# Optimization experiments

Hardware: AMD Instinct MI355X
Metric: run time of the kernel (lower is better)

The kernel has to match this reference:

```python
import jax, jax.numpy as jnp
import numpy as np

SEQ, D, HID, C = 512, 768, 128, 5
NENT, SPAN = 128, 16


def setup_inputs() -> dict:
    key = jax.random.key(0)
    ks = jax.random.split(key, 24)
    s = 0.02

    def rn(k, shape, scale=s):
        return jax.random.normal(k, shape, dtype=jnp.float32) * scale

    inp = {
        "encoder_output": rn(ks[0], (1, SEQ, D), 1.0),
        "holder_idxs": jax.random.randint(ks[1], (NENT, SPAN), 0, SEQ, dtype=jnp.int32),
        "target_idxs": jax.random.randint(ks[2], (NENT, SPAN), 0, SEQ, dtype=jnp.int32),
        "exp_idxs": jax.random.randint(ks[3], (NENT, SPAN), 0, SEQ, dtype=jnp.int32),
    }
    names = ["Wh_f", "bh_f", "Wh_b", "bh_b", "Wt_f", "bt_f", "Wt_b", "bt_b",
             "We_f", "be_f", "We_b", "be_b"]
    for n, k in zip(names, ks[4:16]):
        shape = (4 * HID, D) if n.startswith("W") else (4 * HID,)
        inp[n] = rn(k, shape)
    inp["T_he"] = rn(ks[16], (2 * HID, 2 * HID, 2 * HID))
    inp["T_te"] = rn(ks[17], (2 * HID, 2 * HID, 2 * HID))
    inp["T_cls"] = rn(ks[18], (2 * HID, C, 2 * HID))
    return inp


def _lstm_cell_step(x, W_ih, b):
    # Single LSTM step with h0=c0=0 (the torch module feeds seq_len=1 to nn.LSTM,
    # so W_hh @ h0 vanishes; b = b_ih + b_hh). Gate order: i, f, g, o.
    g = x @ W_ih.T + b                         # [n, L, 4H]
    i, f, gg, o = jnp.split(g, 4, axis=-1)
    c = jax.nn.sigmoid(i) * jnp.tanh(gg)
    return jax.nn.sigmoid(o) * jnp.tanh(c)     # h, [n, L, H]


def _lstm_pool(enc_seq, idxs, Wf, bf, Wb, bb):
    toks = enc_seq[idxs]                       # [n, L, D] gather
    h = jnp.concatenate([_lstm_cell_step(toks, Wf, bf),
                         _lstm_cell_step(toks, Wb, bb)], axis=-1)  # [n, L, 2H]
    return h.max(axis=1)                       # max-pool over span -> [n, 2H]


def reference(encoder_output, holder_idxs, target_idxs, exp_idxs,
              Wh_f, bh_f, Wh_b, bh_b, Wt_f, bt_f, Wt_b, bt_b,
              We_f, be_f, We_b, be_b, T_he, T_te, T_cls):
    enc = encoder_output[0]                    # [SEQ, D]
    He = _lstm_pool(enc, holder_idxs, Wh_f, bh_f, Wh_b, bh_b)   # [nh, 2H]
    Te = _lstm_pool(enc, target_idxs, Wt_f, bt_f, Wt_b, bt_b)   # [nt, 2H]
    Ee = _lstm_pool(enc, exp_idxs, We_f, be_f, We_b, be_b)      # [ne, 2H]

    # hep[i,k] = He[i] @ T_he @ Ee[k];  tep[j,k] = Te[j] @ T_te @ Ee[k]
    hep = jnp.einsum('ia,abc,kc->ikb', He, T_he, Ee)            # [nh, ne, 2H]
    tep = jnp.einsum('ja,abc,kc->jkb', Te, T_te, Ee)            # [nt, ne, 2H]
    # pred[i,j,k,m] = tep[j,k] @ T_cls[:,m,:] @ hep[i,k]
    pred = jnp.einsum('jkb,bmc,ikc->ijkm', tep, T_cls, hep)     # [nh, nt, ne, C]
    return pred
```

## Files before the change

kernel.cpp:

```cpp
#include <hip/hip_runtime.h>
#include <hip/hip_bf16.h>
#include <math.h>

#define DIM   768
#define HID   128
#define H2    256
#define NENT  128
#define SPAN  16
#define NCLS  5

#define POOLB_OFF  0
#define HEPB_OFF   196608
#define TEPB_OFF   (HEPB_OFF + 8388608)
#define TCLSB_OFF  (TEPB_OFF + 8388608)
#define WB_OFF     (TCLSB_OFF + 655360)
#define TOKB_OFF   21168128
#define TMP30_OFF  21168128
#define TMP31_OFF  (TMP30_OFF + 16777216)
#define GATESB_OFF 58060800
#define PREDT_OFF  21168128

typedef __attribute__((ext_vector_type(8))) short bf16x8;
typedef __attribute__((ext_vector_type(4))) float f32x4;

__device__ __forceinline__ float sigmoidf_(float x) { return 1.0f / (1.0f + __expf(-x)); }

__device__ __forceinline__ unsigned short f2bf(float x) {
    __hip_bfloat16 h = __float2bfloat16(x);
    return *reinterpret_cast<unsigned short*>(&h);
}
__device__ __forceinline__ float bf2f(unsigned short u) {
    unsigned int v = ((unsigned int)u) << 16;
    float f; __builtin_memcpy(&f, &v, 4); return f;
}

__global__ __launch_bounds__(256)
void prep_kernel(const float* __restrict__ Whf, const float* __restrict__ Whb,
                 const float* __restrict__ Wtf, const float* __restrict__ Wtb,
                 const float* __restrict__ Wef, const float* __restrict__ Web,
                 const float* __restrict__ Tcls, const float* __restrict__ enc,
                 const int* __restrict__ idx_h, const int* __restrict__ idx_t,
                 const int* __restrict__ idx_e,
                 unsigned short* __restrict__ WB, unsigned short* __restrict__ TB,
                 unsigned short* __restrict__ tokB)
{
    const int bb = blockIdx.x;
    const int tid = threadIdx.x;
    if (bb < 1728) {
        int gid = bb * 256 + tid;
        int t2  = gid / 73728;
        int rem = gid % 73728;
        int n   = rem / 192;
        int c4  = rem % 192;
        int gate = n >> 7, j = n & 127;
        int srow = (gate == 0) ? j : (gate == 1) ? 256 + j : 384 + j;
        const float* W = (t2 == 0) ? Whf : (t2 == 1) ? Whb : (t2 == 2) ? Wtf :
                         (t2 == 3) ? Wtb : (t2 == 4) ? Wef : Web;
        float4 v = ((const float4*)(W + srow * DIM))[c4];
        unsigned short* d = WB + ((size_t)(t2 * 384 + n)) * DIM + c4 * 4;
        d[0] = f2bf(v.x); d[1] = f2bf(v.y); d[2] = f2bf(v.z); d[3] = f2bf(v.w);
    } else if (bb < 3008) {
        int idx = (bb - 1728) * 256 + tid;
        int b = idx / (NCLS * H2);
        int r = idx % (NCLS * H2);
        int m = r >> 8, c = r & 255;
        TB[((m << 8) + c) * H2 + b] = f2bf(Tcls[idx]);
    } else {
        int gid = (bb - 3008) * 256 + tid;
        int r  = gid / 192, c4 = gid % 192;
        int type = r >> 11;
        int rem  = r & 2047;
        const int* idx = (type == 0) ? idx_h : (type == 1) ? idx_t : idx_e;
        int row = idx[rem];
        float4 v = ((const float4*)(enc + (size_t)row * DIM))[c4];
        unsigned short h4[4] = { f2bf(v.x), f2bf(v.y), f2bf(v.z), f2bf(v.w) };
        *(uint2*)(tokB + (size_t)r * DIM + c4 * 4) = *(uint2*)h4;
    }
}

__global__ __launch_bounds__(256)
void gates_mfma(const unsigned short* __restrict__ tokB,
                const unsigned short* __restrict__ WB,
                unsigned short* __restrict__ gatesB)
{
    __shared__ unsigned short As[2][128 * 64];
    __shared__ unsigned short Bs[2][128 * 64];
    const int lbid = ((int)blockIdx.x & 7) * 36 + ((int)blockIdx.x >> 3);
    const int type = lbid / 96;
    const int rem  = lbid % 96;
    const int mb0  = (rem / 6) * 128;
    const int nb0  = (rem % 6) * 128;
    const int tid = threadIdx.x;
    const int w = tid >> 6, l = tid & 63;
    const int lr = l & 15, lg = l >> 4;
    const unsigned short* A = tokB + (size_t)type * 2048 * DIM + (size_t)mb0 * DIM;
    const unsigned short* B = WB   + (size_t)type * 768  * DIM + (size_t)nb0 * DIM;

    const int sr0 = tid >> 3;
    const int sc  = tid & 7;

    bf16x8 ra[4], rb[4];
    #define LOADT(kt)                                                        \
        {                                                                    \
            const int koff = (kt) * 64 + sc * 8;                             \
            _Pragma("unroll")                                                \
            for (int p = 0; p < 4; ++p) {                                    \
                int rr = sr0 + p * 32;                                       \
                ra[p] = *(const bf16x8*)(A + (size_t)rr * DIM + koff);       \
                rb[p] = *(const bf16x8*)(B + (size_t)rr * DIM + koff);       \
            }                                                                \
        }
    #define WRITET(buf)                                                      \
        {                                                                    \
            _Pragma("unroll")                                                \
            for (int p = 0; p < 4; ++p) {                                    \
                int rr = sr0 + p * 32;                                       \
                int bo = (rr * 128 + sc * 16) ^ ((rr & 7) << 4);             \
                *(bf16x8*)((char*)As[buf] + bo) = ra[p];                     \
                *(bf16x8*)((char*)Bs[buf] + bo) = rb[p];                     \
            }                                                                \
        }

    f32x4 acc[4][4];
    #pragma unroll
    for (int mt = 0; mt < 4; ++mt)
        #pragma unroll
        for (int nt = 0; nt < 4; ++nt) acc[mt][nt] = (f32x4){0.f, 0.f, 0.f, 0.f};

    const int am0 = (w & 1) * 64;
    const int bn0 = (w >> 1) * 64;

    LOADT(0);
    WRITET(0);
    __syncthreads();

    int cur = 0;
    #pragma unroll 1
    for (int kt = 0; kt < 12; ++kt) {
        if (kt + 1 < 12) LOADT(kt + 1);

        #pragma unroll
        for (int ks = 0; ks < 2; ++ks) {
            bf16x8 af[4], bf[4];
            #pragma unroll
            for (int mt = 0; mt < 4; ++mt) {
                int rr = am0 + mt * 16 + lr;
                int bo = (rr * 128 + ks * 64 + lg * 16) ^ ((rr & 7) << 4);
                af[mt] = *(const bf16x8*)((const char*)As[cur] + bo);
            }
            #pragma unroll
            for (int nt = 0; nt < 4; ++nt) {
                int rr = bn0 + nt * 16 + lr;
                int bo = (rr * 128 + ks * 64 + lg * 16) ^ ((rr & 7) << 4);
                bf[nt] = *(const bf16x8*)((const char*)Bs[cur] + bo);
            }
            #pragma unroll
            for (int mt = 0; mt < 4; ++mt)
                #pragma unroll
                for (int nt = 0; nt < 4; ++nt)
                    acc[mt][nt] = __builtin_amdgcn_mfma_f32_16x16x32_bf16(af[mt], bf[nt], acc[mt][nt], 0, 0, 0);
        }

        if (kt + 1 < 12) {
            WRITET(cur ^ 1);
        }
        __syncthreads();
        cur ^= 1;
    }
    #undef LOADT
    #undef WRITET

    unsigned short* C = gatesB + (size_t)type * 2048 * 768 + (size_t)mb0 * 768 + nb0;
    #pragma unroll
    for (int mt = 0; mt < 4; ++mt)
        #pragma unroll
        for (int nt = 0; nt < 4; ++nt)
            #pragma unroll
            for (int r = 0; r < 4; ++r)
                C[(size_t)(am0 + mt * 16 + lg * 4 + r) * 768 + bn0 + nt * 16 + lr] = f2bf(acc[mt][nt][r]);
}

__global__ __launch_bounds__(256)
void pool_epilogue(const unsigned short* __restrict__ gatesB,
                   const float* __restrict__ bhf, const float* __restrict__ bhb,
                   const float* __restrict__ btf, const float* __restrict__ btb,
                   const float* __restrict__ bef, const float* __restrict__ beb,
                   unsigned short* __restrict__ poolB)
{
    const int type = blockIdx.x >> 7;
    const int ent  = blockIdx.x & 127;
    const int tid  = threadIdx.x;
    const int dir  = tid >> 7;
    const int j    = tid & 127;
    const float* Bv = (type == 0) ? (dir ? bhb : bhf)
                    : (type == 1) ? (dir ? btb : btf)
                                  : (dir ? beb : bef);
    const float bi = Bv[j], bg = Bv[2 * HID + j], bo = Bv[3 * HID + j];
    const unsigned short* g0 = gatesB + ((size_t)type * 2048 + ent * 16) * 768 + dir * 384 + j;
    float hmax = -1e30f;
    #pragma unroll
    for (int ll = 0; ll < SPAN; ++ll) {
        const unsigned short* gr = g0 + ll * 768;
        float iv = sigmoidf_(bf2f(gr[0])   + bi);
        float gv = tanhf(   bf2f(gr[128]) + bg);
        float ov = sigmoidf_(bf2f(gr[256]) + bo);
        hmax = fmaxf(hmax, ov * tanhf(iv * gv));
    }
    poolB[(size_t)(type * NENT + ent) * H2 + dir * HID + j] = f2bf(hmax);
}

__global__ __launch_bounds__(256)
void p1_thin(const unsigned short* __restrict__ EeB,
             const float* __restrict__ T0, const float* __restrict__ T1,
             unsigned short* __restrict__ tmp30, unsigned short* __restrict__ tmp31)
{
    __shared__ __align__(16) char smem[32768];
    const int bid = blockIdx.x;
    const int t  = bid >> 10;
    const int b  = (bid >> 2) & 255;
    const int aq = bid & 3;
    const int a0 = aq * 64;
    const float* T = t ? T1 : T0;
    unsigned short* outp = t ? tmp31 : tmp30;
    const int tid = threadIdx.x;
    const int w = tid >> 6, l = tid & 63;
    const int lr = l & 15, lg = l >> 4;

    #pragma unroll
    for (int p = 0; p < 8; ++p) {
        int L = tid + p * 256;
        int row = L >> 5, ch = L & 31;
        const float* src = T + ((size_t)(a0 + row) * 256 + b) * 256 + ch * 8;
        float4 v0 = ((const float4*)src)[0];
        float4 v1 = ((const float4*)src)[1];
        bf16x8 hv; unsigned short* hp = (unsigned short*)&hv;
        hp[0]=f2bf(v0.x); hp[1]=f2bf(v0.y); hp[2]=f2bf(v0.z); hp[3]=f2bf(v0.w);
        hp[4]=f2bf(v1.x); hp[5]=f2bf(v1.y); hp[6]=f2bf(v1.z); hp[7]=f2bf(v1.w);
        int bo = (((ch >> 3) << 13) + row * 128 + ((ch & 7) << 4)) ^ ((row & 7) << 4);
        *(bf16x8*)(smem + bo) = hv;
    }
    __syncthreads();

    const int aw = (w & 1) * 32;
    const int kw = (w >> 1) * 64;
    f32x4 acc[2][4];
    #pragma unroll
    for (int mt = 0; mt < 2; ++mt)
        #pragma unroll
        for (int nt = 0; nt < 4; ++nt) acc[mt][nt] = (f32x4){0.f, 0.f, 0.f, 0.f};

    #pragma unroll
    for (int ks = 0; ks < 8; ++ks) {
        const int cb = ks * 64 + lg * 16;
        bf16x8 af[2], bf[4];
        #pragma unroll
        for (int mt = 0; mt < 2; ++mt) {
            int row = aw + mt * 16 + lr;
            int bo = (((cb >> 7) << 13) + row * 128 + (cb & 127)) ^ ((row & 7) << 4);
            af[mt] = *(const bf16x8*)(smem + bo);
        }
        #pragma unroll
        for (int nt = 0; nt < 4; ++nt)
            bf[nt] = *(const bf16x8*)(EeB + (kw + nt * 16 + lr) * H2 + ks * 32 + lg * 8);
        #pragma unroll
        for (int mt = 0; mt < 2; ++mt)
            #pragma unroll
            for (int nt = 0; nt < 4; ++nt)
                acc[mt][nt] = __builtin_amdgcn_mfma_f32_16x16x32_bf16(af[mt], bf[nt], acc[mt][nt], 0, 0, 0);
    }

    #pragma unroll
    for (int mt = 0; mt < 2; ++mt)
        #pragma unroll
        for (int nt = 0; nt < 4; ++nt)
            #pragma unroll
            for (int r = 0; r < 4; ++r) {
                int a_ = a0 + aw + mt * 16 + lg * 4 + r;
                int k_ = kw + nt * 16 + lr;
                outp[((size_t)b * 256 + a_) * 128 + k_] = f2bf(acc[mt][nt][r]);
            }
}

__global__ __launch_bounds__(512)
void gemm2_mfma(const unsigned short* __restrict__ HeB, const unsigned short* __restrict__ TeB,
                const unsigned short* __restrict__ tmp30, const unsigned short* __restrict__ tmp31,
                unsigned short* __restrict__ hepN, unsigned short* __restrict__ tepN)
{
    __shared__ unsigned short WT[128 * 256];
    const int bid = blockIdx.x;
    const int t = bid >> 8;
    const int b = bid & 255;
    const unsigned short* src = (t ? tmp31 : tmp30) + (size_t)b * 32768;
    const unsigned short* Hx = t ? TeB : HeB;
    unsigned short* outp = (t ? tepN : hepN) + (size_t)b * 16384;
    const int tid = threadIdx.x;
    const int w = tid >> 6, l = tid & 63;
    const int lr = l & 15, lg = l >> 4;

    {
        const int a0 = tid >> 4;
        const int k8 = (tid & 15) * 8;
        #pragma unroll
        for (int it = 0; it < 8; ++it) {
            int aa = it * 32 + a0;
            bf16x8 v = *(const bf16x8*)(src + aa * 128 + k8);
            #pragma unroll
            for (int j = 0; j < 8; ++j) {
                int kk = k8 + j;
                int bo = (kk * 512 + aa * 2) ^ (j << 4);
                *(unsigned short*)((char*)WT + bo) = ((unsigned short*)&v)[j];
            }
        }
    }
    __syncthreads();

    const int kw = (w & 1) * 64;
    const int iw = (w >> 1) * 32;
    f32x4 acc[4][2];
    #pragma unroll
    for (int mt = 0; mt < 4; ++mt)
        #pragma unroll
        for (int nt = 0; nt < 2; ++nt) acc[mt][nt] = (f32x4){0.f, 0.f, 0.f, 0.f};

    #pragma unroll
    for (int ks = 0; ks < 8; ++ks) {
        bf16x8 af[4], bf[2];
        #pragma unroll
        for (int mt = 0; mt < 4; ++mt) {
            int kr = kw + mt * 16 + lr;
            int bo = (kr * 512 + (ks * 32 + lg * 8) * 2) ^ ((kr & 7) << 4);
            af[mt] = *(const bf16x8*)((const char*)WT + bo);
        }
        #pragma unroll
        for (int nt = 0; nt < 2; ++nt)
            bf[nt] = *(const bf16x8*)(Hx + (iw + nt * 16 + lr) * H2 + ks * 32 + lg * 8);
        #pragma unroll
        for (int mt = 0; mt < 4; ++mt)
            #pragma unroll
            for (int nt = 0; nt < 2; ++nt)
                acc[mt][nt] = __builtin_amdgcn_mfma_f32_16x16x32_bf16(af[mt], bf[nt], acc[mt][nt], 0, 0, 0);
    }
    #pragma unroll
    for (int mt = 0; mt < 4; ++mt)
        #pragma unroll
        for (int nt = 0; nt < 2; ++nt)
            #pragma unroll
            for (int r = 0; r < 4; ++r) {
                int k_ = kw + mt * 16 + lg * 4 + r;
                int i_ = iw + nt * 16 + lr;
                outp[k_ * 128 + i_] = f2bf(acc[mt][nt][r]);
            }
}

__global__ __launch_bounds__(512)
void step3_mfma(const unsigned short* __restrict__ hepN,
                const unsigned short* __restrict__ tepN,
                const unsigned short* __restrict__ TclsB,
                float* __restrict__ predT)
{
    __shared__ unsigned short hepS[128 * 256];
    __shared__ unsigned short tepS[64 * 256];
    __shared__ unsigned short WS[64 * 256];
    const int lbid = (blockIdx.x & 7) * 32 + (blockIdx.x >> 3);
    const int k  = lbid >> 1;
    const int jh = lbid & 1;
    const int tid = threadIdx.x;
    const int w  = tid >> 6;
    const int l  = tid & 63;
    const int lr = l & 15;
    const int lg = l >> 4;
    const int swz = (lr & 7) << 4;

    #pragma unroll
    for (int q = 0; q < 4; ++q) {
        int bcol = q * 64 + l;
        bf16x8 v = *(const bf16x8*)(tepN + ((size_t)bcol * 128 + k) * 128 + jh * 64 + w * 8);
        #pragma unroll
        for (int r = 0; r < 8; ++r) {
            int j = w * 8 + r;
            int bo = (j * 512 + bcol * 2) ^ (r << 4);
            *(unsigned short*)((char*)tepS + bo) = ((unsigned short*)&v)[r];
        }
    }
    #pragma unroll
    for (int s = 0; s < 2; ++s)
        #pragma unroll
        for (int q = 0; q < 4; ++q) {
            int bcol = q * 64 + l;
            bf16x8 v = *(const bf16x8*)(hepN + ((size_t)bcol * 128 + k) * 128 + w * 16 + s * 8);
            #pragma unroll
            for (int r = 0; r < 8; ++r) {
                int i = w * 16 + s * 8 + r;
                int bo = (i * 512 + bcol * 2) ^ (r << 4);
                *(unsigned short*)((char*)hepS + bo) = ((unsigned short*)&v)[r];
            }
        }
    __syncthreads();

    bf16x8 ha[8];
    #pragma unroll
    for (int ks = 0; ks < 8; ++ks) {
        int ir = w * 16 + lr;
        int bo = (ir * 512 + (ks * 32 + lg * 8) * 2) ^ ((ir & 7) << 4);
        ha[ks] = *(const bf16x8*)((const char*)hepS + bo);
    }

    #pragma unroll 1
    for (int m = 0; m < NCLS; ++m) {
        {
            const unsigned short* tcm = TclsB + (size_t)m * (H2 * H2);
            f32x4 acc1[4][2];
            #pragma unroll
            for (int jt = 0; jt < 4; ++jt)
                #pragma unroll
                for (int ct = 0; ct < 2; ++ct) acc1[jt][ct] = (f32x4){0.f, 0.f, 0.f, 0.f};

            #pragma unroll
            for (int ks = 0; ks < 8; ++ks) {
                bf16x8 a[4], bb[2];
                #pragma unroll
                for (int jt = 0; jt < 4; ++jt) {
                    int byteoff = ((((jt * 16 + lr) << 8) + ks * 32 + lg * 8) << 1) ^ swz;
                    a[jt] = *(const bf16x8*)((const char*)tepS + byteoff);
                }
                #pragma unroll
                for (int ct = 0; ct < 2; ++ct)
                    bb[ct] = *(const bf16x8*)(tcm + (size_t)(w * 32 + ct * 16 + lr) * H2 + ks * 32 + lg * 8);
                #pragma unroll
                for (int jt = 0; jt < 4; ++jt)
                    #pragma unroll
                    for (int ct = 0; ct < 2; ++ct)
                        acc1[jt][ct] = __builtin_amdgcn_mfma_f32_16x16x32_bf16(a[jt], bb[ct], acc1[jt][ct], 0, 0, 0);
            }
            #pragma unroll
            for (int jt = 0; jt < 4; ++jt)
                #pragma unroll
                for (int ct = 0; ct < 2; ++ct)
                    #pragma unroll
                    for (int r = 0; r < 4; ++r) {
                        int j = jt * 16 + lg * 4 + r;
                        int c = w * 32 + ct * 16 + lr;
                        int byteoff = ((((j << 8) + c)) << 1) ^ ((j & 7) << 4);
                        *(unsigned short*)((char*)WS + byteoff) = f2bf(acc1[jt][ct][r]);
                    }
        }
        __syncthreads();

        {
            f32x4 acc2[4];
            #pragma unroll
            for (int jt = 0; jt < 4; ++jt) acc2[jt] = (f32x4){0.f, 0.f, 0.f, 0.f};

            #pragma unroll
            for (int ks = 0; ks < 8; ++ks) {
                #pragma unroll
                for (int jt = 0; jt < 4; ++jt) {
                    int byteoff = ((((jt * 16 + lr) << 8) + ks * 32 + lg * 8) << 1) ^ swz;
                    bf16x8 wb = *(const bf16x8*)((const char*)WS + byteoff);
                    acc2[jt] = __builtin_amdgcn_mfma_f32_16x16x32_bf16(ha[ks], wb, acc2[jt], 0, 0, 0);
                }
            }
            float* po = predT + (size_t)(k * NCLS + m) * (NENT * NENT);
            #pragma unroll
            for (int jt = 0; jt < 4; ++jt)
                #pragma unroll
                for (int r = 0; r < 4; ++r) {
                    int i = w * 16 + lg * 4 + r;
                    int j = jh * 64 + jt * 16 + lr;
                    po[i * NENT + j] = acc2[jt][r];
                }
        }
        __syncthreads();
    }
}

__global__ __launch_bounds__(256)
void transpose_out(const float* __restrict__ predT, float* __restrict__ out)
{
    __shared__ float Ls[160][33];
    const int bid = blockIdx.x;
    const int ij0 = (bid >> 2) * 32;
    const int km0 = (bid & 3) * 160;
    const int t = threadIdx.x;

    #pragma unroll
    for (int q = 0; q < 20; ++q) {
        int r = (t >> 5) + q * 8;
        int c = t & 31;
        Ls[r][c] = predT[(size_t)(km0 + r) * 16384 + ij0 + c];
    }
    __syncthreads();
    for (int idx = t; idx < 32 * 160; idx += 256) {
        int r = idx / 160, c = idx % 160;
        out[(size_t)(ij0 + r) * 640 + km0 + c] = Ls[c][r];
    }
}

extern "C" void kernel_launch(void* const* d_in, const int* in_sizes, int n_in,
                              void* d_out, int out_size, void* d_ws, size_t ws_size,
                              hipStream_t stream)
{
    (void)in_sizes; (void)n_in; (void)out_size; (void)ws_size;
    const float* enc  = (const float*)d_in[0];
    const int*   hidx = (const int*)d_in[1];
    const int*   tidx = (const int*)d_in[2];
    const int*   eidx = (const int*)d_in[3];
    const float* Whf = (const float*)d_in[4];
    const float* bhf = (const float*)d_in[5];
    const float* Whb = (const float*)d_in[6];
    const float* bhb = (const float*)d_in[7];
    const float* Wtf = (const float*)d_in[8];
    const float* btf = (const float*)d_in[9];
    const float* Wtb = (const float*)d_in[10];
    const float* btb = (const float*)d_in[11];
    const float* Wef = (const float*)d_in[12];
    const float* bef = (const float*)d_in[13];
    const float* Web = (const float*)d_in[14];
    const float* beb = (const float*)d_in[15];
    const float* T_he  = (const float*)d_in[16];
    const float* T_te  = (const float*)d_in[17];
    const float* T_cls = (const float*)d_in[18];

    float* out = (float*)d_out;
    char*  ws  = (char*)d_ws;
    unsigned short* poolB  = (unsigned short*)(ws + POOLB_OFF);
    unsigned short* hepN   = (unsigned short*)(ws + HEPB_OFF);
    unsigned short* tepN   = (unsigned short*)(ws + TEPB_OFF);
    unsigned short* TclsB  = (unsigned short*)(ws + TCLSB_OFF);
    unsigned short* WB     = (unsigned short*)(ws + WB_OFF);
    unsigned short* tokB   = (unsigned short*)(ws + TOKB_OFF);
    unsigned short* tmp30  = (unsigned short*)(ws + TMP30_OFF);
    unsigned short* tmp31  = (unsigned short*)(ws + TMP31_OFF);
    unsigned short* gatesB = (unsigned short*)(ws + GATESB_OFF);
    float*          predT  = (float*)(ws + PREDT_OFF);

    unsigned short* HeB = poolB;
    unsigned short* TeB = poolB + 1 * NENT * H2;
    unsigned short* EeB = poolB + 2 * NENT * H2;

    prep_kernel<<<7616, 256, 0, stream>>>(Whf, Whb, Wtf, Wtb, Wef, Web,
                                          T_cls, enc, hidx, tidx, eidx,
                                          WB, TclsB, tokB);

    gates_mfma<<<288, 256, 0, stream>>>(tokB, WB, gatesB);

    pool_epilogue<<<384, 256, 0, stream>>>(gatesB, bhf, bhb, btf, btb, bef, beb, poolB);

    p1_thin<<<2048, 256, 0, stream>>>(EeB, T_he, T_te, tmp30, tmp31);

    gemm2_mfma<<<512, 512, 0, stream>>>(HeB, TeB, tmp30, tmp31, hepN, tepN);

    step3_mfma<<<256, 512, 0, stream>>>(hepN, tepN, TclsB, predT);

    transpose_out<<<2048, 256, 0, stream>>>(predT, out);
}
```

Baseline: 160.0 us.

## Pre-transpose T tensors to bf16 in spare blocks and serialize he/te chains

The fp32 strided read and bf16 conversion of T_he/T_te move out of the p1 GEMM into a separate transpose pass. That pass is folded into the pool-epilogue kernel (for T_he) and into the first gemm2 launch (for T_te) as extra blocks, so the conversion overlaps with existing work. The p1 kernel now loads contiguous bf16 slabs with larger per-block tiles, and the he and te chains run sequentially through one reused tmp3 buffer to shrink the workspace. In exchange there are extra kernel launches, an extra bf16 write and read of each T tensor, and less parallelism per launch.

```diff
diff --git a/kernel.cpp b/kernel.cpp
--- a/kernel.cpp
+++ b/kernel.cpp
@@ -13,12 +13,13 @@
 #define HEPB_OFF   196608
 #define TEPB_OFF   (HEPB_OFF + 8388608)
 #define TCLSB_OFF  (TEPB_OFF + 8388608)
-#define WB_OFF     (TCLSB_OFF + 655360)
-#define TOKB_OFF   21168128
-#define TMP30_OFF  21168128
-#define TMP31_OFF  (TMP30_OFF + 16777216)
-#define GATESB_OFF 58060800
-#define PREDT_OFF  21168128
+#define S_OFF      17629184
+#define WB_OFF     (S_OFF + 0)
+#define TOKB_OFF   (S_OFF + 3538944)
+#define GATESB_OFF (S_OFF + 12976128)
+#define TMP3_OFF   (S_OFF + 0)
+#define TB_OFF     (S_OFF + 22413312)
+#define PREDT_OFF  (S_OFF + 0)
 
 typedef __attribute__((ext_vector_type(8))) short bf16x8;
 typedef __attribute__((ext_vector_type(4))) float f32x4;
@@ -181,119 +182,150 @@
 }
 
 __global__ __launch_bounds__(256)
-void pool_epilogue(const unsigned short* __restrict__ gatesB,
-                   const float* __restrict__ bhf, const float* __restrict__ bhb,
-                   const float* __restrict__ btf, const float* __restrict__ btb,
-                   const float* __restrict__ bef, const float* __restrict__ beb,
-                   unsigned short* __restrict__ poolB)
-{
-    const int type = blockIdx.x >> 7;
-    const int ent  = blockIdx.x & 127;
-    const int tid  = threadIdx.x;
-    const int dir  = tid >> 7;
-    const int j    = tid & 127;
-    const float* Bv = (type == 0) ? (dir ? bhb : bhf)
-                    : (type == 1) ? (dir ? btb : btf)
-                                  : (dir ? beb : bef);
-    const float bi = Bv[j], bg = Bv[2 * HID + j], bo = Bv[3 * HID + j];
-    const unsigned short* g0 = gatesB + ((size_t)type * 2048 + ent * 16) * 768 + dir * 384 + j;
-    float hmax = -1e30f;
-    #pragma unroll
-    for (int ll = 0; ll < SPAN; ++ll) {
-        const unsigned short* gr = g0 + ll * 768;
-        float iv = sigmoidf_(bf2f(gr[0])   + bi);
-        float gv = tanhf(   bf2f(gr[128]) + bg);
-        float ov = sigmoidf_(bf2f(gr[256]) + bo);
-        hmax = fmaxf(hmax, ov * tanhf(iv * gv));
-    }
-    poolB[(size_t)(type * NENT + ent) * H2 + dir * HID + j] = f2bf(hmax);
-}
-
-__global__ __launch_bounds__(256)
-void p1_thin(const unsigned short* __restrict__ EeB,
-             const float* __restrict__ T0, const float* __restrict__ T1,
-             unsigned short* __restrict__ tmp30, unsigned short* __restrict__ tmp31)
-{
-    __shared__ __align__(16) char smem[32768];
+void poolconv(const unsigned short* __restrict__ gatesB,
+              const float* __restrict__ bhf, const float* __restrict__ bhb,
+              const float* __restrict__ btf, const float* __restrict__ btb,
+              const float* __restrict__ bef, const float* __restrict__ beb,
+              unsigned short* __restrict__ poolB,
+              const float* __restrict__ T0, unsigned short* __restrict__ TB)
+{
+    const int bb = blockIdx.x;
+    const int tid = threadIdx.x;
+    if (bb < 384) {
+        const int type = bb >> 7;
+        const int ent  = bb & 127;
+        const int dir  = tid >> 7;
+        const int j    = tid & 127;
+        const float* Bv = (type == 0) ? (dir ? bhb : bhf)
+                        : (type == 1) ? (dir ? btb : btf)
+                                      : (dir ? beb : bef);
+        const float bi = Bv[j], bg = Bv[2 * HID + j], bo = Bv[3 * HID + j];
+        const unsigned short* g0 = gatesB + ((size_t)type * 2048 + ent * 16) * 768 + dir * 384 + j;
+        float hmax = -1e30f;
+        #pragma unroll
+        for (int ll = 0; ll < SPAN; ++ll) {
+            const unsigned short* gr = g0 + ll * 768;
+            float iv = sigmoidf_(bf2f(gr[0])   + bi);
+            float gv = tanhf(   bf2f(gr[128]) + bg);
+            float ov = sigmoidf_(bf2f(gr[256]) + bo);
+            hmax = fmaxf(hmax, ov * tanhf(iv * gv));
+        }
+        poolB[(size_t)(type * NENT + ent) * H2 + dir * HID + j] = f2bf(hmax);
+    } else {
+        int W0 = (bb - 384) * 256 + tid;
+        #pragma unroll 1
+        for (int it = 0; it < 16; ++it) {
+            int idx = W0 + it * 131072;
+            int a  = idx >> 13;
+            int rr = idx & 8191;
+            int b  = rr >> 5;
+            int c8 = rr & 31;
+            const float* src = T0 + ((size_t)(a * 256 + b) << 8) + c8 * 8;
+            float4 v0 = ((const float4*)src)[0];
+            float4 v1 = ((const float4*)src)[1];
+            bf16x8 hv; unsigned short* hp = (unsigned short*)&hv;
+            hp[0]=f2bf(v0.x); hp[1]=f2bf(v0.y); hp[2]=f2bf(v0.z); hp[3]=f2bf(v0.w);
+            hp[4]=f2bf(v1.x); hp[5]=f2bf(v1.y); hp[6]=f2bf(v1.z); hp[7]=f2bf(v1.w);
+            *(bf16x8*)(TB + (((size_t)(b * 256 + a)) << 8) + c8 * 8) = hv;
+        }
+    }
+}
+
+__global__ __launch_bounds__(512)
+void p1tb(const unsigned short* __restrict__ EeB,
+          const unsigned short* __restrict__ TB,
+          unsigned short* __restrict__ tmp3)
+{
+    __shared__ __align__(16) char smem[65536];
     const int bid = blockIdx.x;
-    const int t  = bid >> 10;
-    const int b  = (bid >> 2) & 255;
-    const int aq = bid & 3;
-    const int a0 = aq * 64;
-    const float* T = t ? T1 : T0;
-    unsigned short* outp = t ? tmp31 : tmp30;
+    const int b  = bid >> 1;
+    const int ah = bid & 1;
+    const unsigned short* src = TB + (((size_t)b * 256 + ah * 128) << 8);
     const int tid = threadIdx.x;
     const int w = tid >> 6, l = tid & 63;
     const int lr = l & 15, lg = l >> 4;
 
     #pragma unroll
-    for (int p = 0; p < 8; ++p) {
-        int L = tid + p * 256;
+    for (int it = 0; it < 8; ++it) {
+        int L = it * 512 + tid;
         int row = L >> 5, ch = L & 31;
-        const float* src = T + ((size_t)(a0 + row) * 256 + b) * 256 + ch * 8;
-        float4 v0 = ((const float4*)src)[0];
-        float4 v1 = ((const float4*)src)[1];
-        bf16x8 hv; unsigned short* hp = (unsigned short*)&hv;
-        hp[0]=f2bf(v0.x); hp[1]=f2bf(v0.y); hp[2]=f2bf(v0.z); hp[3]=f2bf(v0.w);
-        hp[4]=f2bf(v1.x); hp[5]=f2bf(v1.y); hp[6]=f2bf(v1.z); hp[7]=f2bf(v1.w);
-        int bo = (((ch >> 3) << 13) + row * 128 + ((ch & 7) << 4)) ^ ((row & 7) << 4);
-        *(bf16x8*)(smem + bo) = hv;
+        bf16x8 v = *(const bf16x8*)(src + (size_t)L * 8);
+        int bo = (row * 512 + ch * 16) ^ ((row & 7) << 4);
+        *(bf16x8*)(smem + bo) = v;
     }
     __syncthreads();
 
-    const int aw = (w & 1) * 32;
-    const int kw = (w >> 1) * 64;
-    f32x4 acc[2][4];
-    #pragma unroll
-    for (int mt = 0; mt < 2; ++mt)
-        #pragma unroll
-        for (int nt = 0; nt < 4; ++nt) acc[mt][nt] = (f32x4){0.f, 0.f, 0.f, 0.f};
+    const int aw = (w & 1) * 64;
+    const int kw = (w >> 1) * 32;
+    f32x4 acc[4][2];
+    #pragma unroll
+    for (int mt = 0; mt < 4; ++mt)
+        #pragma unroll
+        for (int nt = 0; nt < 2; ++nt) acc[mt][nt] = (f32x4){0.f, 0.f, 0.f, 0.f};
 
     #pragma unroll
     for (int ks = 0; ks < 8; ++ks) {
-        const int cb = ks * 64 + lg * 16;
-        bf16x8 af[2], bf[4];
-        #pragma unroll
-        for (int mt = 0; mt < 2; ++mt) {
+        bf16x8 af[4], bf[2];
+        #pragma unroll
+        for (int mt = 0; mt < 4; ++mt) {
             int row = aw + mt * 16 + lr;
-            int bo = (((cb >> 7) << 13) + row * 128 + (cb & 127)) ^ ((row & 7) << 4);
+            int bo = (row * 512 + ks * 64 + lg * 16) ^ ((row & 7) << 4);
             af[mt] = *(const bf16x8*)(smem + bo);
         }
         #pragma unroll
-        for (int nt = 0; nt < 4; ++nt)
+        for (int nt = 0; nt < 2; ++nt)
             bf[nt] = *(const bf16x8*)(EeB + (kw + nt * 16 + lr) * H2 + ks * 32 + lg * 8);
         #pragma unroll
-        for (int mt = 0; mt < 2; ++mt)
-            #pragma unroll
-            for (int nt = 0; nt < 4; ++nt)
+        for (int mt = 0; mt < 4; ++mt)
+            #pragma unroll
+            for (int nt = 0; nt < 2; ++nt)
                 acc[mt][nt] = __builtin_amdgcn_mfma_f32_16x16x32_bf16(af[mt], bf[nt], acc[mt][nt], 0, 0, 0);
     }
 
     #pragma unroll
-    for (int mt = 0; mt < 2; ++mt)
-        #pragma unroll
-        for (int nt = 0; nt < 4; ++nt)
+    for (int mt = 0; mt < 4; ++mt)
+        #pragma unroll
+        for (int nt = 0; nt < 2; ++nt)
             #pragma unroll
             for (int r = 0; r < 4; ++r) {
-                int a_ = a0 + aw + mt * 16 + lg * 4 + r;
+                int a_ = ah * 128 + aw + mt * 16 + lg * 4 + r;
                 int k_ = kw + nt * 16 + lr;
-                outp[((size_t)b * 256 + a_) * 128 + k_] = f2bf(acc[mt][nt][r]);
+                tmp3[((size_t)b * 256 + a_) * 128 + k_] = f2bf(acc[mt][nt][r]);
             }
 }
 
 __global__ __launch_bounds__(512)
-void gemm2_mfma(const unsigned short* __restrict__ HeB, const unsigned short* __restrict__ TeB,
-                const unsigned short* __restrict__ tmp30, const unsigned short* __restrict__ tmp31,
-                unsigned short* __restrict__ hepN, unsigned short* __restrict__ tepN)
-{
+void g2conv(const unsigned short* __restrict__ Hx,
+            const unsigned short* __restrict__ tmp3,
+            unsigned short* __restrict__ outp,
+            const float* __restrict__ T1,
+            unsigned short* __restrict__ TB)
+{
+    const int bb = blockIdx.x;
+    const int tid = threadIdx.x;
+    if (bb >= 256) {
+        int W0 = (bb - 256) * 512 + tid;
+        #pragma unroll 1
+        for (int it = 0; it < 8; ++it) {
+            int idx = W0 + it * 262144;
+            int a  = idx >> 13;
+            int rr = idx & 8191;
+            int b  = rr >> 5;
+            int c8 = rr & 31;
+            const float* src = T1 + ((size_t)(a * 256 + b) << 8) + c8 * 8;
+            float4 v0 = ((const float4*)src)[0];
+            float4 v1 = ((const float4*)src)[1];
+            bf16x8 hv; unsigned short* hp = (unsigned short*)&hv;
+            hp[0]=f2bf(v0.x); hp[1]=f2bf(v0.y); hp[2]=f2bf(v0.z); hp[3]=f2bf(v0.w);
+            hp[4]=f2bf(v1.x); hp[5]=f2bf(v1.y); hp[6]=f2bf(v1.z); hp[7]=f2bf(v1.w);
+            *(bf16x8*)(TB + (((size_t)(b * 256 + a)) << 8) + c8 * 8) = hv;
+        }
+        return;
+    }
     __shared__ unsigned short WT[128 * 256];
-    const int bid = blockIdx.x;
-    const int t = bid >> 8;
-    const int b = bid & 255;
-    const unsigned short* src = (t ? tmp31 : tmp30) + (size_t)b * 32768;
-    const unsigned short* Hx = t ? TeB : HeB;
-    unsigned short* outp = (t ? tepN : hepN) + (size_t)b * 16384;
-    const int tid = threadIdx.x;
+    const int b = bb;
+    const unsigned short* src = tmp3 + (size_t)b * 32768;
+    unsigned short* po = outp + (size_t)b * 16384;
     const int w = tid >> 6, l = tid & 63;
     const int lr = l & 15, lg = l >> 4;
 
@@ -348,7 +380,7 @@
             for (int r = 0; r < 4; ++r) {
                 int k_ = kw + mt * 16 + lg * 4 + r;
                 int i_ = iw + nt * 16 + lr;
-                outp[k_ * 128 + i_] = f2bf(acc[mt][nt][r]);
+                po[k_ * 128 + i_] = f2bf(acc[mt][nt][r]);
             }
 }
 
@@ -529,9 +561,9 @@
     unsigned short* TclsB  = (unsigned short*)(ws + TCLSB_OFF);
     unsigned short* WB     = (unsigned short*)(ws + WB_OFF);
     unsigned short* tokB   = (unsigned short*)(ws + TOKB_OFF);
-    unsigned short* tmp30  = (unsigned short*)(ws + TMP30_OFF);
-    unsigned short* tmp31  = (unsigned short*)(ws + TMP31_OFF);
     unsigned short* gatesB = (unsigned short*)(ws + GATESB_OFF);
+    unsigned short* tmp3   = (unsigned short*)(ws + TMP3_OFF);
+    unsigned short* TB     = (unsigned short*)(ws + TB_OFF);
     float*          predT  = (float*)(ws + PREDT_OFF);
 
     unsigned short* HeB = poolB;
@@ -544,11 +576,16 @@
 
     gates_mfma<<<288, 256, 0, stream>>>(tokB, WB, gatesB);
 
-    pool_epilogue<<<384, 256, 0, stream>>>(gatesB, bhf, bhb, btf, btb, bef, beb, poolB);
-
-    p1_thin<<<2048, 256, 0, stream>>>(EeB, T_he, T_te, tmp30, tmp31);
-
-    gemm2_mfma<<<512, 512, 0, stream>>>(HeB, TeB, tmp30, tmp31, hepN, tepN);
+    poolconv<<<896, 256, 0, stream>>>(gatesB, bhf, bhb, btf, btb, bef, beb,
+                                      poolB, T_he, TB);
+
+    p1tb<<<512, 512, 0, stream>>>(EeB, TB, tmp3);
+
+    g2conv<<<768, 512, 0, stream>>>(HeB, tmp3, hepN, T_te, TB);
+
+    p1tb<<<512, 512, 0, stream>>>(EeB, TB, tmp3);
+
+    g2conv<<<256, 512, 0, stream>>>(TeB, tmp3, tepN, (const float*)nullptr, TB);
 
     step3_mfma<<<256, 512, 0, stream>>>(hepN, tepN, TclsB, predT);
 
```

After: 168.7 us. 1.05x slower.
